# Kernel tuning notes

Hardware: AMD Instinct MI355X
Metric: run time of the kernel (lower is better)

The kernel has to match this reference:

```python
import jax, jax.numpy as jnp
import numpy as np

# tanh-approximate GELU, matching F.gelu(..., approximate='tanh')
_SQRT_2_OVER_PI = 0.7978845608028654

def gelu_tanh(x):
    return 0.5 * x * (1.0 + jnp.tanh(_SQRT_2_OVER_PI * (x + 0.044715 * x * x * x)))

def setup_inputs() -> dict:
    key = jax.random.key(0)
    k1, k2, k3 = jax.random.split(key, 3)
    E, T, H, F = 8, 2048, 1024, 4096
    x = jax.random.normal(k1, (E, T, H), dtype=jnp.float32)
    w1 = jax.random.normal(k2, (E, H, F), dtype=jnp.float32) * (1.0 / np.sqrt(H))
    w2 = jax.random.normal(k3, (E, F, H), dtype=jnp.float32) * (1.0 / np.sqrt(F))
    return {"x": x, "w1": w1, "w2": w2}

def reference(x, w1, w2):
    # [E,T,H] @ [E,H,F] -> [E,T,F]
    h = jnp.einsum('eth,ehf->etf', x, w1)
    h = gelu_tanh(h)
    # [E,T,F] @ [E,F,H] -> [E,T,H]
    return jnp.einsum('etf,efh->eth', h, w2)
```

## Files before the change

kernel.cpp:

```cpp
#include <hip/hip_runtime.h>
#include <hip/hip_bf16.h>

typedef __attribute__((ext_vector_type(8))) short short8;
typedef __attribute__((ext_vector_type(4))) float f32x4;

typedef const __attribute__((address_space(1))) void* as1cv_t;
typedef __attribute__((address_space(3))) void* as3v_t;
typedef __attribute__((address_space(3))) const char* as3cc_t;
typedef __attribute__((address_space(3))) const short8* as3s8_t;

__device__ __forceinline__ unsigned short f2bf(float f) {
    unsigned u = __float_as_uint(f);
    u += 0x7fffu + ((u >> 16) & 1u);
    return (unsigned short)(u >> 16);
}

__device__ __forceinline__ float gelu_tanh_f(float x) {
    float t = 0.7978845608028654f * (x + 0.044715f * x * x * x);
    float u = 2.0f * t;
    u = fminf(fmaxf(u, -30.0f), 30.0f);
    float e = __expf(u);
    float th = (e - 1.0f) / (e + 1.0f);
    return 0.5f * x * (1.0f + th);
}

__global__ void cvt_f32_to_bf16(const float* __restrict__ in,
                                unsigned short* __restrict__ out,
                                long long n) {
    long long i = (long long)blockIdx.x * blockDim.x + threadIdx.x;
    long long stride = (long long)gridDim.x * blockDim.x;
    const float4* in4 = (const float4*)in;
    ushort4* out4 = (ushort4*)out;
    long long n4 = n >> 2;
    for (long long j = i; j < n4; j += stride) {
        float4 v = in4[j];
        ushort4 o;
        o.x = f2bf(v.x); o.y = f2bf(v.y); o.z = f2bf(v.z); o.w = f2bf(v.w);
        out4[j] = o;
    }
}

__global__ void transpose_cvt64(const float* __restrict__ in,
                                unsigned short* __restrict__ out,
                                int R, int C) {
    __shared__ float t[64][65];
    int e = blockIdx.z;
    int c0 = blockIdx.x * 64;
    int r0 = blockIdx.y * 64;
    const float* ine = in + (size_t)e * R * C;
    unsigned short* oute = out + (size_t)e * R * C;
    int tid = threadIdx.x;
    int lx = tid & 15, ly = tid >> 4;
#pragma unroll
    for (int i = 0; i < 4; i++) {
        float4 v = *(const float4*)(ine + (size_t)(r0 + ly + i * 16) * C + c0 + lx * 4);
        t[lx * 4 + 0][ly + i * 16] = v.x;
        t[lx * 4 + 1][ly + i * 16] = v.y;
        t[lx * 4 + 2][ly + i * 16] = v.z;
        t[lx * 4 + 3][ly + i * 16] = v.w;
    }
    __syncthreads();
#pragma unroll
    for (int i = 0; i < 4; i++) {
        int c = ly + i * 16;
        ushort4 o;
        o.x = f2bf(t[c][lx * 4 + 0]);
        o.y = f2bf(t[c][lx * 4 + 1]);
        o.z = f2bf(t[c][lx * 4 + 2]);
        o.w = f2bf(t[c][lx * 4 + 3]);
        *(ushort4*)(oute + (size_t)(c0 + c) * R + r0 + lx * 4) = o;
    }
}

__device__ __forceinline__ void gload16(const void* g, void* l) {
    __builtin_amdgcn_global_load_lds((as1cv_t)g, (as3v_t)l, 16, 0, 0);
}

template <int DO_GELU>
__global__ __launch_bounds__(512, 2) void gemm256p(
    const unsigned short* __restrict__ A,
    const unsigned short* __restrict__ Bt,
    void* __restrict__ Cout,
    int M, int N, int K, int tiles_m, int per_e, int nwg)
{
    int bid = blockIdx.x;
    int gbid = (bid & 7) * (nwg >> 3) + (bid >> 3);
    int e  = gbid / per_e;
    int t0_ = gbid % per_e;
    int bn = t0_ / tiles_m;
    int bm = t0_ % tiles_m;

    const unsigned short* Ae = A  + (size_t)e * M * K + (size_t)bm * 256 * K;
    const unsigned short* Be = Bt + (size_t)e * N * K + (size_t)bn * 256 * K;

    __shared__ alignas(16) unsigned short lds[4 * 16384];
    char* ldsc = (char*)lds;
    as3cc_t lbase = (as3cc_t)(const char*)lds;

    int tid  = threadIdx.x;
    int wid  = tid >> 6;
    int lane = tid & 63;
    int wave_m = wid >> 2;
    int wave_n = wid & 3;

    int c0 = wid * 64 + lane;
    int r0 = c0 >> 2;
    int kb = ((c0 & 3) << 4) ^ (((r0 >> 1) & 3) << 4);
    const char* gA0 = (const char*)(Ae + (size_t)r0 * K) + kb;
    const char* gA1 = (const char*)(Ae + (size_t)(r0 + 128) * K) + kb;
    const char* gB0 = (const char*)(Be + (size_t)r0 * K) + kb;
    const char* gB1 = (const char*)(Be + (size_t)(r0 + 128) * K) + kb;
    int sA = wid << 10;

    int xk = (((lane & 15) >> 1) & 3) << 4;
    unsigned a_off = (wave_m * 128 + (lane & 15)) * 64 + ((((lane >> 4) << 4)) ^ xk);
    unsigned b_off = 16384u + (wave_n * 64 + (lane & 15)) * 64 + ((((lane >> 4) << 4)) ^ xk);

    f32x4 acc[8][4];
    f32x4 zero = {0.0f, 0.0f, 0.0f, 0.0f};
#pragma unroll
    for (int i = 0; i < 8; i++)
#pragma unroll
        for (int j = 0; j < 4; j++) acc[i][j] = zero;

    int NT = K >> 5;

#define STAGE_A(dst) do { \
        gload16(gA0, ldsc + (dst) + sA); \
        gload16(gA1, ldsc + (dst) + 8192 + sA); \
        gA0 += 64; gA1 += 64; } while (0)
#define STAGE_B(dst) do { \
        gload16(gB0, ldsc + (dst) + 16384 + sA); \
        gload16(gB1, ldsc + (dst) + 24576 + sA); \
        gB0 += 64; gB1 += 64; } while (0)

    STAGE_A(0); STAGE_B(0);
    STAGE_A(32768); STAGE_B(32768);
    asm volatile("s_waitcnt vmcnt(4)" ::: "memory");
    __builtin_amdgcn_s_barrier();

    for (int kt = 0; kt < NT; ++kt) {
        unsigned bufT = (unsigned)(kt & 3) << 15;
        unsigned bufS = (unsigned)((kt + 2) & 3) << 15;
        bool more = (kt + 2) < NT;

        as3cc_t pa = lbase + (bufT + a_off);
        as3cc_t pb = lbase + (bufT + b_off);

        short8 af[4], bf[4];
#pragma unroll
        for (int n = 0; n < 4; ++n) bf[n] = *(as3s8_t)(pb + n * 1024);
#pragma unroll
        for (int m = 0; m < 4; ++m) af[m] = *(as3s8_t)(pa + m * 1024);
        if (more) STAGE_A(bufS);
        __builtin_amdgcn_s_barrier();
        asm volatile("s_waitcnt lgkmcnt(0)" ::: "memory");
        __builtin_amdgcn_s_setprio(1);
#pragma unroll
        for (int m = 0; m < 4; ++m)
#pragma unroll
            for (int n = 0; n < 4; ++n)
                acc[m][n] = __builtin_amdgcn_mfma_f32_16x16x32_bf16(af[m], bf[n], acc[m][n], 0, 0, 0);
        __builtin_amdgcn_s_setprio(0);
        __builtin_amdgcn_s_barrier();

#pragma unroll
        for (int m = 0; m < 4; ++m) af[m] = *(as3s8_t)(pa + (m + 4) * 1024);
        if (more) STAGE_B(bufS);
        if (more)              asm volatile("s_waitcnt vmcnt(4)" ::: "memory");
        else if (kt + 1 < NT)  asm volatile("s_waitcnt vmcnt(0)" ::: "memory");
        __builtin_amdgcn_s_barrier();
        asm volatile("s_waitcnt lgkmcnt(0)" ::: "memory");
        __builtin_amdgcn_s_setprio(1);
#pragma unroll
        for (int m = 0; m < 4; ++m)
#pragma unroll
            for (int n = 0; n < 4; ++n)
                acc[m + 4][n] = __builtin_amdgcn_mfma_f32_16x16x32_bf16(af[m], bf[n], acc[m + 4][n], 0, 0, 0);
        __builtin_amdgcn_s_setprio(0);
        __builtin_amdgcn_s_barrier();
    }
#undef STAGE_A
#undef STAGE_B

    int row0 = bm * 256 + wave_m * 128 + ((lane >> 4) << 2);
    int col0 = bn * 256 + wave_n * 64 + (lane & 15);
    if (DO_GELU) {
        unsigned short* Ce = (unsigned short*)Cout + (size_t)e * M * N;
#pragma unroll
        for (int m = 0; m < 8; ++m)
#pragma unroll
            for (int n = 0; n < 4; ++n)
#pragma unroll
                for (int j = 0; j < 4; ++j) {
                    int row = row0 + m * 16 + j;
                    int col = col0 + n * 16;
                    Ce[(size_t)row * N + col] = f2bf(gelu_tanh_f(acc[m][n][j]));
                }
    } else {
        float* Ce = (float*)Cout + (size_t)e * M * N;
#pragma unroll
        for (int m = 0; m < 8; ++m)
#pragma unroll
            for (int n = 0; n < 4; ++n)
#pragma unroll
                for (int j = 0; j < 4; ++j) {
                    int row = row0 + m * 16 + j;
                    int col = col0 + n * 16;
                    Ce[(size_t)row * N + col] = acc[m][n][j];
                }
    }
}

extern "C" void kernel_launch(void* const* d_in, const int* in_sizes, int n_in,
                              void* d_out, int out_size, void* d_ws, size_t ws_size,
                              hipStream_t stream) {
    const float* x  = (const float*)d_in[0];
    const float* w1 = (const float*)d_in[1];
    const float* w2 = (const float*)d_in[2];
    float* out = (float*)d_out;

    const int E = 8, T = 2048, H = 1024, F = 4096;

    unsigned short* xb  = (unsigned short*)d_ws;
    unsigned short* w1t = xb  + (size_t)E * T * H;
    unsigned short* w2t = w1t + (size_t)E * H * F;
    unsigned short* hb  = w2t + (size_t)E * F * H;

    cvt_f32_to_bf16<<<2048, 256, 0, stream>>>(x, xb, (long long)E * T * H);

    transpose_cvt64<<<dim3(F / 64, H / 64, E), 256, 0, stream>>>(w1, w1t, H, F);
    transpose_cvt64<<<dim3(H / 64, F / 64, E), 256, 0, stream>>>(w2, w2t, F, H);

    {
        int M = T, N = F, K = H;
        int tiles_m = M / 256, per_e = tiles_m * (N / 256);
        int nwg = E * per_e;
        gemm256p<1><<<nwg, 512, 0, stream>>>(xb, w1t, hb, M, N, K, tiles_m, per_e, nwg);
    }
    {
        int M = T, N = H, K = F;
        int tiles_m = M / 256, per_e = tiles_m * (N / 256);
        int nwg = E * per_e;
        gemm256p<0><<<nwg, 512, 0, stream>>>(hb, w2t, out, M, N, K, tiles_m, per_e, nwg);
    }
}
```

Before: 414.3 us.

## Shrink GEMM tile to 256x128 with double-buffered LDS and higher occupancy

Replaces the 256x256 block tile (4-stage LDS ring, 8x4 accumulators per wave) with a 256x128 tile using a simple two-buffer LDS pipeline and 4x4 accumulators per wave. The launch bound rises from 2 to 4 blocks per CU, and the grid doubles. The aim is more resident waves and more workgroups to hide latency, at the cost of lower operand reuse per tile. The new pipeline also waits for all outstanding loads (vmcnt(0)) each iteration, which loses the deeper prefetch the old schedule had.

```diff
diff --git a/kernel.cpp b/kernel.cpp
--- a/kernel.cpp
+++ b/kernel.cpp
@@ -77,7 +77,7 @@
 }
 
 template <int DO_GELU>
-__global__ __launch_bounds__(512, 2) void gemm256p(
+__global__ __launch_bounds__(512, 4) void gemm256x128(
     const unsigned short* __restrict__ A,
     const unsigned short* __restrict__ Bt,
     void* __restrict__ Cout,
@@ -91,17 +91,17 @@
     int bm = t0_ % tiles_m;
 
     const unsigned short* Ae = A  + (size_t)e * M * K + (size_t)bm * 256 * K;
-    const unsigned short* Be = Bt + (size_t)e * N * K + (size_t)bn * 256 * K;
-
-    __shared__ alignas(16) unsigned short lds[4 * 16384];
+    const unsigned short* Be = Bt + (size_t)e * N * K + (size_t)bn * 128 * K;
+
+    __shared__ alignas(16) unsigned short lds[2 * 12288];
     char* ldsc = (char*)lds;
     as3cc_t lbase = (as3cc_t)(const char*)lds;
 
     int tid  = threadIdx.x;
     int wid  = tid >> 6;
     int lane = tid & 63;
-    int wave_m = wid >> 2;
-    int wave_n = wid & 3;
+    int wave_m = wid >> 1;
+    int wave_n = wid & 1;
 
     int c0 = wid * 64 + lane;
     int r0 = c0 >> 2;
@@ -109,52 +109,47 @@
     const char* gA0 = (const char*)(Ae + (size_t)r0 * K) + kb;
     const char* gA1 = (const char*)(Ae + (size_t)(r0 + 128) * K) + kb;
     const char* gB0 = (const char*)(Be + (size_t)r0 * K) + kb;
-    const char* gB1 = (const char*)(Be + (size_t)(r0 + 128) * K) + kb;
     int sA = wid << 10;
 
     int xk = (((lane & 15) >> 1) & 3) << 4;
-    unsigned a_off = (wave_m * 128 + (lane & 15)) * 64 + ((((lane >> 4) << 4)) ^ xk);
-    unsigned b_off = 16384u + (wave_n * 64 + (lane & 15)) * 64 + ((((lane >> 4) << 4)) ^ xk);
-
-    f32x4 acc[8][4];
+    unsigned a_off = (unsigned)((wave_m * 64 + (lane & 15)) * 64 + ((((lane >> 4) << 4)) ^ xk));
+    unsigned b_off = 16384u + (unsigned)((wave_n * 64 + (lane & 15)) * 64 + ((((lane >> 4) << 4)) ^ xk));
+
+    f32x4 acc[4][4];
     f32x4 zero = {0.0f, 0.0f, 0.0f, 0.0f};
 #pragma unroll
-    for (int i = 0; i < 8; i++)
+    for (int i = 0; i < 4; i++)
 #pragma unroll
         for (int j = 0; j < 4; j++) acc[i][j] = zero;
 
     int NT = K >> 5;
 
-#define STAGE_A(dst) do { \
+#define STAGE(dst) do { \
         gload16(gA0, ldsc + (dst) + sA); \
         gload16(gA1, ldsc + (dst) + 8192 + sA); \
-        gA0 += 64; gA1 += 64; } while (0)
-#define STAGE_B(dst) do { \
         gload16(gB0, ldsc + (dst) + 16384 + sA); \
-        gload16(gB1, ldsc + (dst) + 24576 + sA); \
-        gB0 += 64; gB1 += 64; } while (0)
-
-    STAGE_A(0); STAGE_B(0);
-    STAGE_A(32768); STAGE_B(32768);
-    asm volatile("s_waitcnt vmcnt(4)" ::: "memory");
+        gA0 += 64; gA1 += 64; gB0 += 64; } while (0)
+
+    STAGE(0);
+    asm volatile("s_waitcnt vmcnt(0)" ::: "memory");
     __builtin_amdgcn_s_barrier();
 
     for (int kt = 0; kt < NT; ++kt) {
-        unsigned bufT = (unsigned)(kt & 3) << 15;
-        unsigned bufS = (unsigned)((kt + 2) & 3) << 15;
-        bool more = (kt + 2) < NT;
-
-        as3cc_t pa = lbase + (bufT + a_off);
-        as3cc_t pb = lbase + (bufT + b_off);
+        unsigned bufC = (unsigned)(kt & 1) * 24576u;
+        unsigned bufN = (unsigned)(~kt & 1) * 24576u;
+        bool more = (kt + 1) < NT;
+
+        if (more) STAGE(bufN);
+
+        as3cc_t pa = lbase + (bufC + a_off);
+        as3cc_t pb = lbase + (bufC + b_off);
 
         short8 af[4], bf[4];
 #pragma unroll
         for (int n = 0; n < 4; ++n) bf[n] = *(as3s8_t)(pb + n * 1024);
 #pragma unroll
         for (int m = 0; m < 4; ++m) af[m] = *(as3s8_t)(pa + m * 1024);
-        if (more) STAGE_A(bufS);
-        __builtin_amdgcn_s_barrier();
-        asm volatile("s_waitcnt lgkmcnt(0)" ::: "memory");
+
         __builtin_amdgcn_s_setprio(1);
 #pragma unroll
         for (int m = 0; m < 4; ++m)
@@ -162,33 +157,18 @@
             for (int n = 0; n < 4; ++n)
                 acc[m][n] = __builtin_amdgcn_mfma_f32_16x16x32_bf16(af[m], bf[n], acc[m][n], 0, 0, 0);
         __builtin_amdgcn_s_setprio(0);
+
+        if (more) asm volatile("s_waitcnt vmcnt(0)" ::: "memory");
         __builtin_amdgcn_s_barrier();
-
-#pragma unroll
-        for (int m = 0; m < 4; ++m) af[m] = *(as3s8_t)(pa + (m + 4) * 1024);
-        if (more) STAGE_B(bufS);
-        if (more)              asm volatile("s_waitcnt vmcnt(4)" ::: "memory");
-        else if (kt + 1 < NT)  asm volatile("s_waitcnt vmcnt(0)" ::: "memory");
-        __builtin_amdgcn_s_barrier();
-        asm volatile("s_waitcnt lgkmcnt(0)" ::: "memory");
-        __builtin_amdgcn_s_setprio(1);
-#pragma unroll
-        for (int m = 0; m < 4; ++m)
-#pragma unroll
-            for (int n = 0; n < 4; ++n)
-                acc[m + 4][n] = __builtin_amdgcn_mfma_f32_16x16x32_bf16(af[m], bf[n], acc[m + 4][n], 0, 0, 0);
-        __builtin_amdgcn_s_setprio(0);
-        __builtin_amdgcn_s_barrier();
-    }
-#undef STAGE_A
-#undef STAGE_B
-
-    int row0 = bm * 256 + wave_m * 128 + ((lane >> 4) << 2);
-    int col0 = bn * 256 + wave_n * 64 + (lane & 15);
+    }
+#undef STAGE
+
+    int row0 = bm * 256 + wave_m * 64 + ((lane >> 4) << 2);
+    int col0 = bn * 128 + wave_n * 64 + (lane & 15);
     if (DO_GELU) {
         unsigned short* Ce = (unsigned short*)Cout + (size_t)e * M * N;
 #pragma unroll
-        for (int m = 0; m < 8; ++m)
+        for (int m = 0; m < 4; ++m)
 #pragma unroll
             for (int n = 0; n < 4; ++n)
 #pragma unroll
@@ -200,7 +180,7 @@
     } else {
         float* Ce = (float*)Cout + (size_t)e * M * N;
 #pragma unroll
-        for (int m = 0; m < 8; ++m)
+        for (int m = 0; m < 4; ++m)
 #pragma unroll
             for (int n = 0; n < 4; ++n)
 #pragma unroll
@@ -234,14 +214,14 @@
 
     {
         int M = T, N = F, K = H;
-        int tiles_m = M / 256, per_e = tiles_m * (N / 256);
+        int tiles_m = M / 256, per_e = tiles_m * (N / 128);
         int nwg = E * per_e;
-        gemm256p<1><<<nwg, 512, 0, stream>>>(xb, w1t, hb, M, N, K, tiles_m, per_e, nwg);
+        gemm256x128<1><<<nwg, 512, 0, stream>>>(xb, w1t, hb, M, N, K, tiles_m, per_e, nwg);
     }
     {
         int M = T, N = H, K = F;
-        int tiles_m = M / 256, per_e = tiles_m * (N / 256);
+        int tiles_m = M / 256, per_e = tiles_m * (N / 128);
         int nwg = E * per_e;
-        gemm256p<0><<<nwg, 512, 0, stream>>>(hb, w2t, out, M, N, K, tiles_m, per_e, nwg);
-    }
-}
+        gemm256x128<0><<<nwg, 512, 0, stream>>>(hb, w2t, out, M, N, K, tiles_m, per_e, nwg);
+    }
+}
```

After: 432.8 us. +4.5%, slower.

## Restructure bf16 GEMM mainloop into 64-deep K tiles with four-phase ping-pong schedule

Applied to the files above, without the earlier changes.

The GEMM mainloop now processes K in 64-element steps instead of 32, using two 64 KB LDS buffers in place of four 32 KB ones. It uses a new XOR swizzle with 128-byte rows. Each iteration is split into four MFMA quadrants (AL×BL, AL×BH, AH×BH, AH×BL). Fragment loads and the global→LDS staging of the next A and B halves are interleaved between barriers, with sched_barrier fences and raised priority around the MFMA blocks. The intent is to halve the barrier and waitcnt overhead per unit of K and to overlap memory traffic with matrix math more evenly, at the cost of more barriers per iteration and more fragile scheduling.

```diff
diff --git a/kernel.cpp b/kernel.cpp
--- a/kernel.cpp
+++ b/kernel.cpp
@@ -76,8 +76,10 @@
     __builtin_amdgcn_global_load_lds((as1cv_t)g, (as3v_t)l, 16, 0, 0);
 }
 
+#define MFMA_BF16 __builtin_amdgcn_mfma_f32_16x16x32_bf16
+
 template <int DO_GELU>
-__global__ __launch_bounds__(512, 2) void gemm256p(
+__global__ __launch_bounds__(512, 2) void gemm8p(
     const unsigned short* __restrict__ A,
     const unsigned short* __restrict__ Bt,
     void* __restrict__ Cout,
@@ -90,12 +92,13 @@
     int bn = t0_ / tiles_m;
     int bm = t0_ % tiles_m;
 
-    const unsigned short* Ae = A  + (size_t)e * M * K + (size_t)bm * 256 * K;
-    const unsigned short* Be = Bt + (size_t)e * N * K + (size_t)bn * 256 * K;
-
-    __shared__ alignas(16) unsigned short lds[4 * 16384];
+    const size_t K2 = (size_t)K * 2;
+    const char* Ae = (const char*)A  + ((size_t)e * M * K + (size_t)bm * 256 * K) * 2;
+    const char* Be = (const char*)Bt + ((size_t)e * N * K + (size_t)bn * 256 * K) * 2;
+
+    __shared__ alignas(16) unsigned short lds[2 * 32768];
     char* ldsc = (char*)lds;
-    as3cc_t lbase = (as3cc_t)(const char*)lds;
+    as3cc_t lb = (as3cc_t)(const char*)lds;
 
     int tid  = threadIdx.x;
     int wid  = tid >> 6;
@@ -103,18 +106,21 @@
     int wave_m = wid >> 2;
     int wave_n = wid & 3;
 
-    int c0 = wid * 64 + lane;
-    int r0 = c0 >> 2;
-    int kb = ((c0 & 3) << 4) ^ (((r0 >> 1) & 3) << 4);
-    const char* gA0 = (const char*)(Ae + (size_t)r0 * K) + kb;
-    const char* gA1 = (const char*)(Ae + (size_t)(r0 + 128) * K) + kb;
-    const char* gB0 = (const char*)(Be + (size_t)r0 * K) + kb;
-    const char* gB1 = (const char*)(Be + (size_t)(r0 + 128) * K) + kb;
-    int sA = wid << 10;
-
-    int xk = (((lane & 15) >> 1) & 3) << 4;
-    unsigned a_off = (wave_m * 128 + (lane & 15)) * 64 + ((((lane >> 4) << 4)) ^ xk);
-    unsigned b_off = 16384u + (wave_n * 64 + (lane & 15)) * 64 + ((((lane >> 4) << 4)) ^ xk);
+    int srow = wid * 8 + (lane >> 3);
+    int kbsw = ((lane & 7) ^ (srow & 7)) << 4;
+    const char* gA = Ae + (size_t)srow * K2 + kbsw;
+    const char* gB = Be + (size_t)srow * K2 + kbsw;
+    const size_t HROW = 64 * K2;
+    const size_t HALF = 128 * K2;
+    int sOff = wid << 10;
+
+    unsigned kg   = (unsigned)(lane >> 4);
+    unsigned keyl = (unsigned)(lane & 7) & 7u;
+    keyl = (unsigned)((lane & 15) & 7);
+    unsigned sl0  = (kg ^ keyl) << 4;
+    unsigned aoff = (unsigned)(wave_m * 16384 + (lane & 15) * 128) + sl0;
+    unsigned boff = 32768u + (unsigned)((wave_n >> 1) * 16384 +
+                    ((wave_n & 1) * 64 + (lane & 15)) * 128) + sl0;
 
     f32x4 acc[8][4];
     f32x4 zero = {0.0f, 0.0f, 0.0f, 0.0f};
@@ -123,65 +129,124 @@
 #pragma unroll
         for (int j = 0; j < 4; j++) acc[i][j] = zero;
 
-    int NT = K >> 5;
-
-#define STAGE_A(dst) do { \
-        gload16(gA0, ldsc + (dst) + sA); \
-        gload16(gA1, ldsc + (dst) + 8192 + sA); \
-        gA0 += 64; gA1 += 64; } while (0)
-#define STAGE_B(dst) do { \
-        gload16(gB0, ldsc + (dst) + 16384 + sA); \
-        gload16(gB1, ldsc + (dst) + 24576 + sA); \
-        gB0 += 64; gB1 += 64; } while (0)
-
-    STAGE_A(0); STAGE_B(0);
-    STAGE_A(32768); STAGE_B(32768);
-    asm volatile("s_waitcnt vmcnt(4)" ::: "memory");
+    int NT = K >> 6;
+
+#define STG_A(h, r, bufbit) gload16(gA + (h) * HALF + (r) * HROW, \
+        ldsc + ((bufbit) << 16) + (h) * 16384 + (r) * 8192 + sOff)
+#define STG_B(h, r, bufbit) gload16(gB + (h) * HALF + (r) * HROW, \
+        ldsc + ((bufbit) << 16) + 32768 + (h) * 16384 + (r) * 8192 + sOff)
+
+    STG_A(0, 0, 0); STG_A(0, 1, 0); STG_A(1, 0, 0); STG_A(1, 1, 0);
+    STG_B(0, 0, 0); STG_B(0, 1, 0); STG_B(1, 0, 0); STG_B(1, 1, 0);
+    gB += 128;
+    if (NT > 1) {
+        STG_B(0, 0, 1); STG_B(0, 1, 1); STG_B(1, 0, 1); STG_B(1, 1, 1);
+        asm volatile("s_waitcnt vmcnt(4)" ::: "memory");
+    } else {
+        asm volatile("s_waitcnt vmcnt(0)" ::: "memory");
+    }
+    gB += 128;
+    gA += 128;
     __builtin_amdgcn_s_barrier();
 
-    for (int kt = 0; kt < NT; ++kt) {
-        unsigned bufT = (unsigned)(kt & 3) << 15;
-        unsigned bufS = (unsigned)((kt + 2) & 3) << 15;
-        bool more = (kt + 2) < NT;
-
-        as3cc_t pa = lbase + (bufT + a_off);
-        as3cc_t pb = lbase + (bufT + b_off);
-
-        short8 af[4], bf[4];
-#pragma unroll
-        for (int n = 0; n < 4; ++n) bf[n] = *(as3s8_t)(pb + n * 1024);
-#pragma unroll
-        for (int m = 0; m < 4; ++m) af[m] = *(as3s8_t)(pa + m * 1024);
-        if (more) STAGE_A(bufS);
-        __builtin_amdgcn_s_barrier();
-        asm volatile("s_waitcnt lgkmcnt(0)" ::: "memory");
+    for (int t = 0; t < NT; ++t) {
+        unsigned bufR = (unsigned)(t & 1) << 16;
+        int wbA = (t + 1) & 1;
+        int wbB = t & 1;
+        bool stA = (t + 1) < NT;
+        bool stB = (t + 2) < NT;
+
+        unsigned pa0 = bufR + aoff, pa1 = pa0 ^ 64u;
+        unsigned pb0 = bufR + boff, pb1 = pb0 ^ 64u;
+
+        short8 aL[4][2], aH[4][2], bL[2][2], bH[2][2];
+
+#pragma unroll
+        for (int mi = 0; mi < 4; ++mi) {
+            aL[mi][0] = *(as3s8_t)(lb + (pa0 + mi * 2048));
+            aL[mi][1] = *(as3s8_t)(lb + (pa1 + mi * 2048));
+        }
+#pragma unroll
+        for (int ni = 0; ni < 2; ++ni) {
+            bL[ni][0] = *(as3s8_t)(lb + (pb0 + ni * 2048));
+            bL[ni][1] = *(as3s8_t)(lb + (pb1 + ni * 2048));
+        }
+        if (stA) { STG_A(0, 0, wbA); STG_A(0, 1, wbA); }
+        __builtin_amdgcn_sched_barrier(0);
+        __builtin_amdgcn_s_barrier();
         __builtin_amdgcn_s_setprio(1);
 #pragma unroll
-        for (int m = 0; m < 4; ++m)
-#pragma unroll
-            for (int n = 0; n < 4; ++n)
-                acc[m][n] = __builtin_amdgcn_mfma_f32_16x16x32_bf16(af[m], bf[n], acc[m][n], 0, 0, 0);
+        for (int ks = 0; ks < 2; ++ks)
+#pragma unroll
+            for (int mi = 0; mi < 4; ++mi)
+#pragma unroll
+                for (int ni = 0; ni < 2; ++ni)
+                    acc[mi][ni] = MFMA_BF16(aL[mi][ks], bL[ni][ks], acc[mi][ni], 0, 0, 0);
         __builtin_amdgcn_s_setprio(0);
-        __builtin_amdgcn_s_barrier();
-
-#pragma unroll
-        for (int m = 0; m < 4; ++m) af[m] = *(as3s8_t)(pa + (m + 4) * 1024);
-        if (more) STAGE_B(bufS);
-        if (more)              asm volatile("s_waitcnt vmcnt(4)" ::: "memory");
-        else if (kt + 1 < NT)  asm volatile("s_waitcnt vmcnt(0)" ::: "memory");
-        __builtin_amdgcn_s_barrier();
-        asm volatile("s_waitcnt lgkmcnt(0)" ::: "memory");
+        __builtin_amdgcn_sched_barrier(0);
+        __builtin_amdgcn_s_barrier();
+
+#pragma unroll
+        for (int ni = 0; ni < 2; ++ni) {
+            bH[ni][0] = *(as3s8_t)(lb + (pb0 + (2 + ni) * 2048));
+            bH[ni][1] = *(as3s8_t)(lb + (pb1 + (2 + ni) * 2048));
+        }
+        if (stA) { STG_A(1, 0, wbA); STG_A(1, 1, wbA); }
+        gA += 128;
+        __builtin_amdgcn_sched_barrier(0);
+        __builtin_amdgcn_s_barrier();
         __builtin_amdgcn_s_setprio(1);
 #pragma unroll
-        for (int m = 0; m < 4; ++m)
-#pragma unroll
-            for (int n = 0; n < 4; ++n)
-                acc[m + 4][n] = __builtin_amdgcn_mfma_f32_16x16x32_bf16(af[m], bf[n], acc[m + 4][n], 0, 0, 0);
+        for (int ks = 0; ks < 2; ++ks)
+#pragma unroll
+            for (int mi = 0; mi < 4; ++mi)
+#pragma unroll
+                for (int ni = 0; ni < 2; ++ni)
+                    acc[mi][2 + ni] = MFMA_BF16(aL[mi][ks], bH[ni][ks], acc[mi][2 + ni], 0, 0, 0);
         __builtin_amdgcn_s_setprio(0);
-        __builtin_amdgcn_s_barrier();
-    }
-#undef STAGE_A
-#undef STAGE_B
+        __builtin_amdgcn_sched_barrier(0);
+        __builtin_amdgcn_s_barrier();
+
+#pragma unroll
+        for (int mi = 0; mi < 4; ++mi) {
+            aH[mi][0] = *(as3s8_t)(lb + (pa0 + (4 + mi) * 2048));
+            aH[mi][1] = *(as3s8_t)(lb + (pa1 + (4 + mi) * 2048));
+        }
+        if (stB) { STG_B(0, 0, wbB); STG_B(0, 1, wbB); }
+        __builtin_amdgcn_sched_barrier(0);
+        __builtin_amdgcn_s_barrier();
+        __builtin_amdgcn_s_setprio(1);
+#pragma unroll
+        for (int ks = 0; ks < 2; ++ks)
+#pragma unroll
+            for (int mi = 0; mi < 4; ++mi)
+#pragma unroll
+                for (int ni = 0; ni < 2; ++ni)
+                    acc[4 + mi][2 + ni] = MFMA_BF16(aH[mi][ks], bH[ni][ks], acc[4 + mi][2 + ni], 0, 0, 0);
+        __builtin_amdgcn_s_setprio(0);
+        __builtin_amdgcn_sched_barrier(0);
+        __builtin_amdgcn_s_barrier();
+
+        if (stB) { STG_B(1, 0, wbB); STG_B(1, 1, wbB); }
+        gB += 128;
+        if (stB) asm volatile("s_waitcnt vmcnt(4)" ::: "memory");
+        else     asm volatile("s_waitcnt vmcnt(0)" ::: "memory");
+        __builtin_amdgcn_sched_barrier(0);
+        __builtin_amdgcn_s_barrier();
+        __builtin_amdgcn_s_setprio(1);
+#pragma unroll
+        for (int ks = 0; ks < 2; ++ks)
+#pragma unroll
+            for (int mi = 0; mi < 4; ++mi)
+#pragma unroll
+                for (int ni = 0; ni < 2; ++ni)
+                    acc[4 + mi][ni] = MFMA_BF16(aH[mi][ks], bL[ni][ks], acc[4 + mi][ni], 0, 0, 0);
+        __builtin_amdgcn_s_setprio(0);
+        __builtin_amdgcn_sched_barrier(0);
+        __builtin_amdgcn_s_barrier();
+    }
+#undef STG_A
+#undef STG_B
 
     int row0 = bm * 256 + wave_m * 128 + ((lane >> 4) << 2);
     int col0 = bn * 256 + wave_n * 64 + (lane & 15);
@@ -236,12 +301,12 @@
         int M = T, N = F, K = H;
         int tiles_m = M / 256, per_e = tiles_m * (N / 256);
         int nwg = E * per_e;
-        gemm256p<1><<<nwg, 512, 0, stream>>>(xb, w1t, hb, M, N, K, tiles_m, per_e, nwg);
+        gemm8p<1><<<nwg, 512, 0, stream>>>(xb, w1t, hb, M, N, K, tiles_m, per_e, nwg);
     }
     {
         int M = T, N = H, K = F;
         int tiles_m = M / 256, per_e = tiles_m * (N / 256);
         int nwg = E * per_e;
-        gemm256p<0><<<nwg, 512, 0, stream>>>(hb, w2t, out, M, N, K, tiles_m, per_e, nwg);
-    }
-}
+        gemm8p<0><<<nwg, 512, 0, stream>>>(hb, w2t, out, M, N, K, tiles_m, per_e, nwg);
+    }
+}
```

Result: faster. 389.7 us (-5.9%).
